# Optimization experiments

Measured on AMD Instinct MI355X. Metric: run time of the kernel, lower is better.

Reference implementation:

```python
import jax, jax.numpy as jnp
import numpy as np

TRAIN_ROIS = 200
POS_RATIO = 0.33
POS_MAX = int(TRAIN_ROIS * POS_RATIO)  # 66
BBOX_STD = np.array([0.1, 0.1, 0.2, 0.2], dtype=np.float32)


def _iou(boxes1, boxes2):
    # boxes1 [N,4], boxes2 [G,4] in (y1,x1,y2,x2) -> IoU [N,G]
    b1 = boxes1[:, None, :]
    b2 = boxes2[None, :, :]
    y1 = jnp.maximum(b1[..., 0], b2[..., 0])
    x1 = jnp.maximum(b1[..., 1], b2[..., 1])
    y2 = jnp.minimum(b1[..., 2], b2[..., 2])
    x2 = jnp.minimum(b1[..., 3], b2[..., 3])
    inter = jnp.maximum(x2 - x1, 0.0) * jnp.maximum(y2 - y1, 0.0)
    a1 = (b1[..., 2] - b1[..., 0]) * (b1[..., 3] - b1[..., 1])
    a2 = (b2[..., 2] - b2[..., 0]) * (b2[..., 3] - b2[..., 1])
    union = a1 + a2 - inter
    return inter / jnp.where(union > 0, union, 1.0)


def _box_refine(box, gt):
    # standard Mask R-CNN box_refinement_graph
    h = box[..., 2] - box[..., 0]
    w = box[..., 3] - box[..., 1]
    cy = box[..., 0] + 0.5 * h
    cx = box[..., 1] + 0.5 * w
    gh = gt[..., 2] - gt[..., 0]
    gw = gt[..., 3] - gt[..., 1]
    gcy = gt[..., 0] + 0.5 * gh
    gcx = gt[..., 1] + 0.5 * gw
    return jnp.stack([(gcy - cy) / h, (gcx - cx) / w,
                      jnp.log(gh / h), jnp.log(gw / w)], axis=-1)


def _per_image(proposals, gt_boxes, gt_captions, scores):
    T = TRAIN_ROIS
    valid_p = jnp.sum(jnp.abs(proposals), axis=1) > 0   # trim_zeros on proposals
    valid_g = jnp.sum(jnp.abs(gt_boxes), axis=1) > 0    # trim_zeros on gt
    # IoU only feeds comparisons/argmax (pure index selection) -> no grad path
    overlaps = jax.lax.stop_gradient(_iou(proposals, gt_boxes))
    overlaps = jnp.where(valid_g[None, :], overlaps, -1.0)
    roi_iou_max = jnp.max(overlaps, axis=1)
    pos_bool = valid_p & (roi_iou_max >= 0.5)
    neg_bool = valid_p & (roi_iou_max < 0.5)
    # deterministic stand-in for tf.random.shuffle[:count]: first `count` in index order
    pos_idx = jnp.where(pos_bool, size=POS_MAX, fill_value=0)[0]
    pos_cnt = jnp.minimum(jnp.sum(pos_bool), POS_MAX)
    pos_valid = jnp.arange(POS_MAX) < pos_cnt
    neg_target = (pos_cnt.astype(jnp.float32) / POS_RATIO).astype(jnp.int32) - pos_cnt
    neg_idx = jnp.where(neg_bool, size=T, fill_value=0)[0]
    neg_cnt = jnp.minimum(jnp.minimum(neg_target, jnp.sum(neg_bool)), T - pos_cnt)
    neg_valid = jnp.arange(T) < neg_cnt

    positive_rois = proposals[pos_idx]                  # [POS_MAX,4]
    negative_rois = proposals[neg_idx]                  # [T,4]
    gt_assign = jnp.argmax(overlaps[pos_idx], axis=1)   # [POS_MAX]
    roi_gt_boxes = gt_boxes[gt_assign]
    roi_gt_captions = gt_captions[gt_assign]
    roi_gt_scores = scores[gt_assign]
    # for padded (invalid) positive slots, use the roi itself -> zero, finite deltas
    safe_gt = jnp.where(pos_valid[:, None], roi_gt_boxes, positive_rois)
    deltas = _box_refine(positive_rois, safe_gt) / jnp.asarray(BBOX_STD)

    # positives occupy slots [0,pos_cnt), negatives [pos_cnt, pos_cnt+neg_cnt), rest zero-padded
    pos_slots = jnp.where(pos_valid, jnp.arange(POS_MAX), T)   # T is out-of-range -> dropped
    neg_slots = jnp.where(neg_valid, pos_cnt + jnp.arange(T), T)
    rois = (jnp.zeros((T, 4), proposals.dtype)
            .at[pos_slots].set(positive_rois, mode='drop')
            .at[neg_slots].set(negative_rois, mode='drop'))
    out_deltas = jnp.zeros((T, 4), proposals.dtype).at[pos_slots].set(deltas, mode='drop')
    out_caps = jnp.zeros((T, gt_captions.shape[1]), gt_captions.dtype).at[pos_slots].set(roi_gt_captions, mode='drop')
    out_scores = jnp.zeros((T,), scores.dtype).at[pos_slots].set(roi_gt_scores, mode='drop')
    return rois, out_deltas, out_caps, out_scores


def setup_inputs() -> dict:
    key = jax.random.key(0)
    B, N, G = 8, 4096, 512
    k1, k2, k3, k4, k5 = jax.random.split(key, 5)
    c = jax.random.uniform(k1, (B, N, 2))                   # box centers (y,x)
    s = jax.random.uniform(k2, (B, N, 2)) * 0.2 + 0.02      # box sizes
    lo = jnp.clip(c - 0.5 * s, 0.0, 1.0)
    hi = jnp.clip(c + 0.5 * s, 0.0, 1.0)
    proposals = jnp.concatenate([lo, hi], axis=-1)          # (y1,x1,y2,x2)
    # gt boxes = perturbed copies of first G proposals (ensures IoU>=0.5 positives exist)
    p = proposals[:, :G, :] + jax.random.normal(k3, (B, G, 4)) * 0.02
    y1 = jnp.minimum(p[..., 0], p[..., 2]); y2 = jnp.maximum(p[..., 0], p[..., 2]) + 1e-3
    x1 = jnp.minimum(p[..., 1], p[..., 3]); x2 = jnp.maximum(p[..., 1], p[..., 3]) + 1e-3
    gt_boxes = jnp.clip(jnp.stack([y1, x1, y2, x2], axis=-1), 0.0, 1.0)
    # exercise the zero-trim logic: zero-pad tails
    proposals = proposals.at[:, N - 256:, :].set(0.0)
    gt_boxes = gt_boxes.at[:, G - 32:, :].set(0.0)
    gt_captions = jax.random.randint(k4, (B, G, 15), 0, 10000, dtype=jnp.int32)
    scores = jax.random.uniform(k5, (B, G))
    return {"proposals": proposals, "gt_boxes": gt_boxes,
            "gt_captions": gt_captions, "scores": scores}


def reference(proposals, gt_boxes, gt_captions, scores):
    return jax.vmap(_per_image)(proposals, gt_boxes, gt_captions, scores)
```

## Files before the change

kernel.cpp:

```cpp
#include <hip/hip_runtime.h>
#include <math.h>

#define BB   8
#define NP   4096
#define NG   512
#define TT   200
#define PMAX 66

#define CH   8
#define PB   32
#define NBLK (NP / PB)

__global__ __launch_bounds__(256) void iou_phase(
    const float* __restrict__ proposals, const float* __restrict__ gt,
    int* __restrict__ argj, unsigned int* __restrict__ posmask,
    unsigned int* __restrict__ negmask) {
#pragma clang fp contract(off)
  const int b     = blockIdx.x >> 7;
  const int blk   = blockIdx.x & 127;
  const int pbase = blk * PB;

  __shared__ float4 sgt[NG];
  __shared__ short  sidx[NG];
  __shared__ int    s_wcnt[4];
  __shared__ float  rbest[CH][PB];
  __shared__ int    ridx[CH][PB];

  const int tid  = threadIdx.x;
  const int wave = tid >> 6;
  const int lane = tid & 63;

  const int plocal  = tid & (PB - 1);
  const int chunkid = tid >> 5;
  const int i       = pbase + plocal;

  const float4 p = ((const float4*)proposals)[(size_t)b * NP + i];

  const float4* gtb4 = (const float4*)(gt + (size_t)b * NG * 4);
  const int ja = wave * 128 + lane;
  const int jb = ja + 64;
  const float4 ga = gtb4[ja];
  const float4 gb = gtb4[jb];
  const bool va = (fabsf(ga.x) + fabsf(ga.y) + fabsf(ga.z) + fabsf(ga.w)) > 0.0f;
  const bool vb = (fabsf(gb.x) + fabsf(gb.y) + fabsf(gb.z) + fabsf(gb.w)) > 0.0f;
  const unsigned long long ma = __ballot(va);
  const unsigned long long mb = __ballot(vb);
  if (lane == 0) s_wcnt[wave] = __popcll(ma) + __popcll(mb);
  __syncthreads();

  int wbase = 0;
  for (int w = 0; w < 4; ++w) if (w < wave) wbase += s_wcnt[w];
  const int nv = s_wcnt[0] + s_wcnt[1] + s_wcnt[2] + s_wcnt[3];

  const unsigned long long lower = (1ull << lane) - 1ull;
  if (va) {
    int k = wbase + __popcll(ma & lower);
    sgt[k] = ga; sidx[k] = (short)ja;
  }
  if (vb) {
    int k = wbase + __popcll(ma) + __popcll(mb & lower);
    sgt[k] = gb; sidx[k] = (short)jb;
  }
  __syncthreads();

  const float a1  = (p.z - p.x) * (p.w - p.y);
  const int   csz = (nv + CH - 1) / CH;
  int j0 = chunkid * csz;
  int j1 = j0 + csz; if (j1 > nv) j1 = nv;
  if (j0 > nv) j0 = nv;

  float best = -INFINITY;
  int bk = 0;
  for (int j = j0; j < j1; ++j) {
    float4 g = sgt[j];
    float y1 = fmaxf(p.x, g.x);
    float x1 = fmaxf(p.y, g.y);
    float y2 = fminf(p.z, g.z);
    float x2 = fminf(p.w, g.w);
    float inter = fmaxf(x2 - x1, 0.0f) * fmaxf(y2 - y1, 0.0f);
    float a2 = (g.z - g.x) * (g.w - g.y);
    float un = a1 + a2 - inter;
    float iou = inter / (un > 0.0f ? un : 1.0f);
    if (iou > best) { best = iou; bk = j; }
  }
  rbest[chunkid][plocal] = best;
  ridx[chunkid][plocal]  = bk;
  __syncthreads();

  if (tid < PB) {
    float bb = rbest[0][tid];
    int   bi = ridx[0][tid];
    for (int c = 1; c < CH; ++c) {
      float v = rbest[c][tid];
      if (v > bb) { bb = v; bi = ridx[c][tid]; }
    }
    int borig = (int)sidx[bi];
    bool vp  = (fabsf(p.x) + fabsf(p.y) + fabsf(p.z) + fabsf(p.w)) > 0.0f;
    bool isp = vp && (bb >= 0.5f);
    bool isn = vp && (bb <  0.5f);
    unsigned long long mp = __ballot(isp);
    unsigned long long mn = __ballot(isn);
    argj[(size_t)b * NP + i] = borig;
    if (tid == 0) {
      posmask[(size_t)b * NBLK + blk] = (unsigned int)mp;
      negmask[(size_t)b * NBLK + blk] = (unsigned int)mn;
    }
  }
}

__global__ __launch_bounds__(256) void select_phase(
    const float* __restrict__ proposals, const float* __restrict__ gt,
    const int* __restrict__ caps, const float* __restrict__ scores,
    const int* __restrict__ argj, const unsigned int* __restrict__ posmask,
    const unsigned int* __restrict__ negmask, float* __restrict__ out) {
#pragma clang fp contract(off)
  const int b = blockIdx.x;

  __shared__ int s_pos[PMAX];
  __shared__ int s_neg[TT];
  __shared__ int s_tot[2];

  const int tid  = threadIdx.x;
  const int wave = tid >> 6;
  const int lane = tid & 63;

  if (wave < 2) {
    const unsigned int* msk = (wave == 0 ? posmask : negmask) + (size_t)b * NBLK;
    const int cap = (wave == 0) ? PMAX : TT;
    int* list = (wave == 0) ? s_pos : s_neg;
    unsigned int m0 = msk[2 * lane];
    unsigned int m1 = msk[2 * lane + 1];
    int cnt = __popc(m0) + __popc(m1);
    int incl = cnt;
    for (int d = 1; d < 64; d <<= 1) {
      int u = __shfl_up(incl, d, 64);
      if (lane >= d) incl += u;
    }
    int base = incl - cnt;
    if (lane == 63) s_tot[wave] = incl;
    while (m0 && base < cap) {
      int bit = __ffs(m0) - 1;
      list[base] = lane * 64 + bit;
      m0 &= m0 - 1; ++base;
    }
    int base1 = base + ((base < cap) ? 0 : 0);
    while (m1 && base1 < cap) {
      int bit = __ffs(m1) - 1;
      list[base1] = lane * 64 + 32 + bit;
      m1 &= m1 - 1; ++base1;
    }
  }
  __syncthreads();

  const int pos_total = s_tot[0];
  const int neg_total = s_tot[1];
  int pos_cnt = pos_total < PMAX ? pos_total : PMAX;
  int neg_cnt = (int)((float)pos_cnt / 0.33f) - pos_cnt;
  if (neg_total < neg_cnt)    neg_cnt = neg_total;
  if (TT - pos_cnt < neg_cnt) neg_cnt = TT - pos_cnt;
  if (neg_cnt < 0)            neg_cnt = 0;

  float* rois   = out + (size_t)b * TT * 4;
  float* deltas = out + (size_t)BB * TT * 4 + (size_t)b * TT * 4;
  float* ocaps  = out + (size_t)2 * BB * TT * 4 + (size_t)b * TT * 15;
  float* osc    = out + (size_t)2 * BB * TT * 4 + (size_t)BB * TT * 15 + (size_t)b * TT;

  const int k = tid;
  if (k < TT) {
    if (k < pos_cnt) {
      int i = s_pos[k];
      const float* pp = proposals + ((size_t)b * NP + i) * 4;
      float p0 = pp[0], p1 = pp[1], p2 = pp[2], p3 = pp[3];
      int g = argj[(size_t)b * NP + i];
      const float* gg = gt + ((size_t)b * NG + g) * 4;
      float g0 = gg[0], g1 = gg[1], g2 = gg[2], g3 = gg[3];

      rois[k * 4 + 0] = p0; rois[k * 4 + 1] = p1;
      rois[k * 4 + 2] = p2; rois[k * 4 + 3] = p3;

      float h  = p2 - p0, ww = p3 - p1;
      float cy = p0 + 0.5f * h, cx = p1 + 0.5f * ww;
      float gh = g2 - g0, gw = g3 - g1;
      float gcy = g0 + 0.5f * gh, gcx = g1 + 0.5f * gw;
      deltas[k * 4 + 0] = ((gcy - cy) / h) / 0.1f;
      deltas[k * 4 + 1] = ((gcx - cx) / ww) / 0.1f;
      deltas[k * 4 + 2] = logf(gh / h) / 0.2f;
      deltas[k * 4 + 3] = logf(gw / ww) / 0.2f;

      const int* cp = caps + ((size_t)b * NG + g) * 15;
      for (int c = 0; c < 15; ++c) ocaps[k * 15 + c] = (float)cp[c];
      osc[k] = scores[(size_t)b * NG + g];
    } else {
      if (k < pos_cnt + neg_cnt) {
        int i = s_neg[k - pos_cnt];
        const float* pp = proposals + ((size_t)b * NP + i) * 4;
        rois[k * 4 + 0] = pp[0]; rois[k * 4 + 1] = pp[1];
        rois[k * 4 + 2] = pp[2]; rois[k * 4 + 3] = pp[3];
      } else {
        rois[k * 4 + 0] = 0.0f; rois[k * 4 + 1] = 0.0f;
        rois[k * 4 + 2] = 0.0f; rois[k * 4 + 3] = 0.0f;
      }
      deltas[k * 4 + 0] = 0.0f; deltas[k * 4 + 1] = 0.0f;
      deltas[k * 4 + 2] = 0.0f; deltas[k * 4 + 3] = 0.0f;
      for (int c = 0; c < 15; ++c) ocaps[k * 15 + c] = 0.0f;
      osc[k] = 0.0f;
    }
  }
}

extern "C" void kernel_launch(void* const* d_in, const int* in_sizes, int n_in,
                              void* d_out, int out_size, void* d_ws, size_t ws_size,
                              hipStream_t stream) {
  const float* proposals = (const float*)d_in[0];
  const float* gt        = (const float*)d_in[1];
  const int*   caps      = (const int*)d_in[2];
  const float* scores    = (const float*)d_in[3];
  float* out = (float*)d_out;

  char* ws = (char*)d_ws;
  int*          argj = (int*)ws;
  unsigned int* pm   = (unsigned int*)(ws + (size_t)BB * NP * 4);
  unsigned int* nm   = pm + (size_t)BB * NBLK;

  hipLaunchKernelGGL(iou_phase, dim3(BB * NBLK), dim3(256), 0, stream,
                     proposals, gt, argj, pm, nm);
  hipLaunchKernelGGL(select_phase, dim3(BB), dim3(256), 0, stream,
                     proposals, gt, caps, scores, argj, pm, nm, out);
}
```

Baseline: 80.24 us.

## Process two proposals per thread and skip IoU for all-zero proposal blocks

Each iou_phase block now covers 64 proposals instead of 32. Every thread computes IoU for two proposals against the same gt box loaded from shared memory, which halves the shared-memory loads and gt-area computations per IoU. Blocks whose proposals are all zero-padded skip the IoU loop entirely, and the pos/neg masks become 64-bit words, which simplifies the compaction in select_phase. In exchange the grid is half as large (512 blocks), which lowers parallelism, and each thread uses more registers.

```diff
diff --git a/kernel.cpp b/kernel.cpp
--- a/kernel.cpp
+++ b/kernel.cpp
@@ -8,33 +8,34 @@
 #define PMAX 66
 
 #define CH   8
-#define PB   32
-#define NBLK (NP / PB)
+#define NB64 (NP / 64)
 
 __global__ __launch_bounds__(256) void iou_phase(
     const float* __restrict__ proposals, const float* __restrict__ gt,
-    int* __restrict__ argj, unsigned int* __restrict__ posmask,
-    unsigned int* __restrict__ negmask) {
+    int* __restrict__ argj, unsigned long long* __restrict__ posmask,
+    unsigned long long* __restrict__ negmask) {
 #pragma clang fp contract(off)
-  const int b     = blockIdx.x >> 7;
-  const int blk   = blockIdx.x & 127;
-  const int pbase = blk * PB;
+  const int b     = blockIdx.x >> 6;
+  const int blk   = blockIdx.x & 63;
+  const int pbase = blk * 64;
 
   __shared__ float4 sgt[NG];
   __shared__ short  sidx[NG];
   __shared__ int    s_wcnt[4];
-  __shared__ float  rbest[CH][PB];
-  __shared__ int    ridx[CH][PB];
+  __shared__ float  rbest[CH][64];
+  __shared__ int    ridx[CH][64];
 
   const int tid  = threadIdx.x;
   const int wave = tid >> 6;
   const int lane = tid & 63;
 
-  const int plocal  = tid & (PB - 1);
+  const int plocal  = tid & 31;
   const int chunkid = tid >> 5;
-  const int i       = pbase + plocal;
-
-  const float4 p = ((const float4*)proposals)[(size_t)b * NP + i];
+  const int ip      = pbase + plocal;
+  const int iq      = ip + 32;
+
+  const float4 p = ((const float4*)proposals)[(size_t)b * NP + ip];
+  const float4 q = ((const float4*)proposals)[(size_t)b * NP + iq];
 
   const float4* gtb4 = (const float4*)(gt + (size_t)b * NG * 4);
   const int ja = wave * 128 + lane;
@@ -63,31 +64,53 @@
   }
   __syncthreads();
 
-  const float a1  = (p.z - p.x) * (p.w - p.y);
+  const float a1p = (p.z - p.x) * (p.w - p.y);
+  const float a1q = (q.z - q.x) * (q.w - q.y);
   const int   csz = (nv + CH - 1) / CH;
   int j0 = chunkid * csz;
   int j1 = j0 + csz; if (j1 > nv) j1 = nv;
   if (j0 > nv) j0 = nv;
 
-  float best = -INFINITY;
-  int bk = 0;
-  for (int j = j0; j < j1; ++j) {
-    float4 g = sgt[j];
-    float y1 = fmaxf(p.x, g.x);
-    float x1 = fmaxf(p.y, g.y);
-    float y2 = fminf(p.z, g.z);
-    float x2 = fminf(p.w, g.w);
-    float inter = fmaxf(x2 - x1, 0.0f) * fmaxf(y2 - y1, 0.0f);
-    float a2 = (g.z - g.x) * (g.w - g.y);
-    float un = a1 + a2 - inter;
-    float iou = inter / (un > 0.0f ? un : 1.0f);
-    if (iou > best) { best = iou; bk = j; }
-  }
-  rbest[chunkid][plocal] = best;
-  ridx[chunkid][plocal]  = bk;
-  __syncthreads();
-
-  if (tid < PB) {
+  const bool vpp = (fabsf(p.x) + fabsf(p.y) + fabsf(p.z) + fabsf(p.w)) > 0.0f;
+  const bool vpq = (fabsf(q.x) + fabsf(q.y) + fabsf(q.z) + fabsf(q.w)) > 0.0f;
+  const bool any_valid = __ballot(vpp || vpq) != 0ull;
+
+  float bestp = -INFINITY, bestq = -INFINITY;
+  int bkp = 0, bkq = 0;
+  if (any_valid) {
+#pragma unroll 2
+    for (int j = j0; j < j1; ++j) {
+      float4 g = sgt[j];
+      float a2 = (g.z - g.x) * (g.w - g.y);
+      {
+        float y1 = fmaxf(p.x, g.x);
+        float x1 = fmaxf(p.y, g.y);
+        float y2 = fminf(p.z, g.z);
+        float x2 = fminf(p.w, g.w);
+        float inter = fmaxf(x2 - x1, 0.0f) * fmaxf(y2 - y1, 0.0f);
+        float un = a1p + a2 - inter;
+        float iou = inter / (un > 0.0f ? un : 1.0f);
+        if (iou > bestp) { bestp = iou; bkp = j; }
+      }
+      {
+        float y1 = fmaxf(q.x, g.x);
+        float x1 = fmaxf(q.y, g.y);
+        float y2 = fminf(q.z, g.z);
+        float x2 = fminf(q.w, g.w);
+        float inter = fmaxf(x2 - x1, 0.0f) * fmaxf(y2 - y1, 0.0f);
+        float un = a1q + a2 - inter;
+        float iou = inter / (un > 0.0f ? un : 1.0f);
+        if (iou > bestq) { bestq = iou; bkq = j; }
+      }
+    }
+  }
+  rbest[chunkid][plocal]      = bestp;
+  ridx[chunkid][plocal]       = bkp;
+  rbest[chunkid][plocal + 32] = bestq;
+  ridx[chunkid][plocal + 32]  = bkq;
+  __syncthreads();
+
+  if (tid < 64) {
     float bb = rbest[0][tid];
     int   bi = ridx[0][tid];
     for (int c = 1; c < CH; ++c) {
@@ -95,15 +118,16 @@
       if (v > bb) { bb = v; bi = ridx[c][tid]; }
     }
     int borig = (int)sidx[bi];
-    bool vp  = (fabsf(p.x) + fabsf(p.y) + fabsf(p.z) + fabsf(p.w)) > 0.0f;
+    const float4 mine = (tid < 32) ? p : q;
+    bool vp  = (fabsf(mine.x) + fabsf(mine.y) + fabsf(mine.z) + fabsf(mine.w)) > 0.0f;
     bool isp = vp && (bb >= 0.5f);
     bool isn = vp && (bb <  0.5f);
     unsigned long long mp = __ballot(isp);
     unsigned long long mn = __ballot(isn);
-    argj[(size_t)b * NP + i] = borig;
+    argj[(size_t)b * NP + pbase + tid] = borig;
     if (tid == 0) {
-      posmask[(size_t)b * NBLK + blk] = (unsigned int)mp;
-      negmask[(size_t)b * NBLK + blk] = (unsigned int)mn;
+      posmask[(size_t)b * NB64 + blk] = mp;
+      negmask[(size_t)b * NB64 + blk] = mn;
     }
   }
 }
@@ -111,8 +135,8 @@
 __global__ __launch_bounds__(256) void select_phase(
     const float* __restrict__ proposals, const float* __restrict__ gt,
     const int* __restrict__ caps, const float* __restrict__ scores,
-    const int* __restrict__ argj, const unsigned int* __restrict__ posmask,
-    const unsigned int* __restrict__ negmask, float* __restrict__ out) {
+    const int* __restrict__ argj, const unsigned long long* __restrict__ posmask,
+    const unsigned long long* __restrict__ negmask, float* __restrict__ out) {
 #pragma clang fp contract(off)
   const int b = blockIdx.x;
 
@@ -125,12 +149,12 @@
   const int lane = tid & 63;
 
   if (wave < 2) {
-    const unsigned int* msk = (wave == 0 ? posmask : negmask) + (size_t)b * NBLK;
+    const unsigned long long* msk =
+        (wave == 0 ? posmask : negmask) + (size_t)b * NB64;
     const int cap = (wave == 0) ? PMAX : TT;
     int* list = (wave == 0) ? s_pos : s_neg;
-    unsigned int m0 = msk[2 * lane];
-    unsigned int m1 = msk[2 * lane + 1];
-    int cnt = __popc(m0) + __popc(m1);
+    unsigned long long m = msk[lane];
+    int cnt = __popcll(m);
     int incl = cnt;
     for (int d = 1; d < 64; d <<= 1) {
       int u = __shfl_up(incl, d, 64);
@@ -138,16 +162,10 @@
     }
     int base = incl - cnt;
     if (lane == 63) s_tot[wave] = incl;
-    while (m0 && base < cap) {
-      int bit = __ffs(m0) - 1;
+    while (m && base < cap) {
+      int bit = __ffsll((unsigned long long)m) - 1;
       list[base] = lane * 64 + bit;
-      m0 &= m0 - 1; ++base;
-    }
-    int base1 = base + ((base < cap) ? 0 : 0);
-    while (m1 && base1 < cap) {
-      int bit = __ffs(m1) - 1;
-      list[base1] = lane * 64 + 32 + bit;
-      m1 &= m1 - 1; ++base1;
+      m &= m - 1; ++base;
     }
   }
   __syncthreads();
@@ -218,11 +236,11 @@
   float* out = (float*)d_out;
 
   char* ws = (char*)d_ws;
-  int*          argj = (int*)ws;
-  unsigned int* pm   = (unsigned int*)(ws + (size_t)BB * NP * 4);
-  unsigned int* nm   = pm + (size_t)BB * NBLK;
-
-  hipLaunchKernelGGL(iou_phase, dim3(BB * NBLK), dim3(256), 0, stream,
+  int*                argj = (int*)ws;
+  unsigned long long* pm   = (unsigned long long*)(ws + (size_t)BB * NP * 4);
+  unsigned long long* nm   = pm + (size_t)BB * NB64;
+
+  hipLaunchKernelGGL(iou_phase, dim3(BB * NB64), dim3(256), 0, stream,
                      proposals, gt, argj, pm, nm);
   hipLaunchKernelGGL(select_phase, dim3(BB), dim3(256), 0, stream,
                      proposals, gt, caps, scores, argj, pm, nm, out);
```

Result: no change. 79.64 us (-0.8%).
